# Kernel tuning notes

Hardware: AMD Instinct MI355X
Metric: run time of the kernel (lower is better)

## Reference

```python
import jax, jax.numpy as jnp
import numpy as np

HIDDEN = 2560
HEADS = 32
HEAD_DIM = HIDDEN // HEADS  # 80


def setup_inputs() -> dict:
    key = jax.random.key(0)
    ks = jax.random.split(key, 7)
    B, S, L = 2, 2048, 512
    scale = 1.0 / np.sqrt(HIDDEN)
    return {
        "hidden_states": jax.random.normal(ks[0], (B, S, HIDDEN), jnp.float32),
        "live_state": jax.random.normal(ks[1], (B, L, HIDDEN), jnp.float32),
        # nn.Linear weights stored [out, in]; y = x @ W.T
        "Wq": jax.random.normal(ks[2], (HIDDEN, HIDDEN), jnp.float32) * scale,
        "Wk": jax.random.normal(ks[3], (HIDDEN, HIDDEN), jnp.float32) * scale,
        "Wv": jax.random.normal(ks[4], (HIDDEN, HIDDEN), jnp.float32) * scale,
        "Wo": jax.random.normal(ks[5], (HIDDEN, HIDDEN), jnp.float32) * scale,
        "gate_param": jax.random.normal(ks[6], (), jnp.float32) * 0.1,
    }


def reference(hidden_states, live_state, Wq, Wk, Wv, Wo, gate_param):
    B, S, D = hidden_states.shape
    L = live_state.shape[1]
    H, Dh = HEADS, HEAD_DIM

    q = (hidden_states @ Wq.T).reshape(B, S, H, Dh).transpose(0, 2, 1, 3)  # [B,H,S,Dh]
    k = (live_state @ Wk.T).reshape(B, L, H, Dh).transpose(0, 2, 1, 3)    # [B,H,L,Dh]
    v = (live_state @ Wv.T).reshape(B, L, H, Dh).transpose(0, 2, 1, 3)    # [B,H,L,Dh]

    scale = 1.0 / np.sqrt(Dh)
    scores = jnp.einsum("bhsd,bhld->bhsl", q, k) * scale
    attn_weights = jax.nn.softmax(scores, axis=-1)                        # [B,H,S,L]
    attn_out = jnp.einsum("bhsl,bhld->bhsd", attn_weights, v)
    attn_out = attn_out.transpose(0, 2, 1, 3).reshape(B, S, D)
    attn_out = attn_out @ Wo.T

    gate = jnp.tanh(gate_param)
    output = gate * attn_out
    return output, attn_weights
```

## Files before the change

### kernel.cpp

```cpp
#include <hip/hip_runtime.h>
#include <hip/hip_fp16.h>
#include <cstdint>
#include <cstddef>

#define HID 2560
#define NH  32
#define DHD 80
#define DHP 96
#define NB  2
#define NS  2048
#define NL  512

typedef _Float16 half8_t __attribute__((ext_vector_type(8)));
typedef float f32x4_t __attribute__((ext_vector_type(4)));

__device__ __forceinline__ void gload_lds16(const __half* g, __half* l) {
  __builtin_amdgcn_global_load_lds(
      (const __attribute__((address_space(1))) unsigned int*)g,
      (__attribute__((address_space(3))) unsigned int*)l, 16, 0, 0);
}

__global__ __launch_bounds__(256) void cast_all(const float* __restrict__ X,
                                                const float* __restrict__ LS,
                                                const float* __restrict__ Wq,
                                                const float* __restrict__ Wk,
                                                const float* __restrict__ Wv,
                                                const float* __restrict__ Wo,
                                                __half* __restrict__ Xh,
                                                __half* __restrict__ Lh,
                                                __half* __restrict__ Wqh,
                                                __half* __restrict__ Wkh,
                                                __half* __restrict__ Wvh,
                                                __half* __restrict__ Woh,
                                                __half* __restrict__ Qa,
                                                __half* __restrict__ Ka) {
  const int nX = NB * NS * HID / 4, nL = NB * NL * HID / 4, nW = HID * HID / 4;
  const int ncast = nX + nL + 4 * nW;
  const int qrows = NB * NH * NS, krows = NB * NH * NL;
  const int total = ncast + qrows + krows;
  for (int i = blockIdx.x * 256 + threadIdx.x; i < total; i += gridDim.x * 256) {
    if (i < ncast) {
      const float* src; __half* dst; int off;
      if (i < nX) { src = X; dst = Xh; off = i; }
      else if (i < nX + nL) { src = LS; dst = Lh; off = i - nX; }
      else {
        int j = i - nX - nL;
        int w = j / nW; off = j - w * nW;
        src = (w == 0) ? Wq : (w == 1) ? Wk : (w == 2) ? Wv : Wo;
        dst = (w == 0) ? Wqh : (w == 1) ? Wkh : (w == 2) ? Wvh : Woh;
      }
      float4 v = ((const float4*)src)[off];
      union { __half h[4]; uint2 u; } r;
      r.h[0] = __float2half(v.x);
      r.h[1] = __float2half(v.y);
      r.h[2] = __float2half(v.z);
      r.h[3] = __float2half(v.w);
      ((uint2*)dst)[off] = r.u;
    } else {
      const int j = i - ncast;
      const uint4 z = {0, 0, 0, 0};
      uint4* p = (j < qrows)
          ? (uint4*)(Qa + (size_t)j * DHP + DHD)
          : (uint4*)(Ka + (size_t)(j - qrows) * DHP + DHD);
      p[0] = z; p[1] = z;
    }
  }
}

__device__ __forceinline__ void gemm256_core(const __half* A, const __half* Bt,
                                             int bm, int bn, __half* smem,
                                             f32x4_t (&acc)[8][4]) {
  const int K = HID;
  const int tid  = threadIdx.x;
  const int lane = tid & 63;
  const int wave = tid >> 6;
  const int wr = wave >> 2, wc = wave & 3;
  const int fr = lane & 15, kb = lane >> 4;

  const int sr = tid >> 3;
  const int sj = (tid & 7) ^ (sr & 7);
  const __half* gA = A  + (size_t)(bm * 256 + sr) * K + sj * 8;
  const __half* gB = Bt + (size_t)(bn * 256 + sr) * K + sj * 8;

  auto stage = [&](int h, int kt, int bank) {
    const __half* gbase = (h < 2) ? gA : gB;
    const int rbase = (h & 1) * 128;
#pragma unroll
    for (int i = 0; i < 2; ++i) {
      const __half* g = gbase + (size_t)(rbase + i * 64) * K + (size_t)kt * 64;
      __half* l = smem + bank * 32768 + (h < 2 ? 0 : 16384) + (rbase + i * 64) * 64 + tid * 8;
      gload_lds16(g, l);
    }
  };
  auto rdA = [&](int m, int kk, int bank) -> half8_t {
    const int row = wr * 128 + m * 16 + fr;
    const int off = row * 128 + ((kk * 64 + kb * 16) ^ ((fr & 7) << 4));
    return *(const half8_t*)((const char*)(smem + bank * 32768) + off);
  };
  auto rdB = [&](int n, int kk, int bank) -> half8_t {
    const int row = wc * 64 + n * 16 + fr;
    const int off = row * 128 + ((kk * 64 + kb * 16) ^ ((fr & 7) << 4));
    return *(const half8_t*)((const char*)(smem + bank * 32768 + 16384) + off);
  };

  half8_t af[4][2], bf[4][2];

#pragma unroll
  for (int h = 0; h < 4; ++h) stage(h, 0, 0);

  const int nk = K >> 6;
  for (int kt = 0; kt < nk; ++kt) {
    const int bk = kt & 1, nb2 = bk ^ 1;
    const bool pf = (kt + 1 < nk);

    if (pf) { stage(0, kt + 1, nb2); stage(1, kt + 1, nb2); }
    if (pf) asm volatile("s_waitcnt vmcnt(4)" ::: "memory");
    else    asm volatile("s_waitcnt vmcnt(0)" ::: "memory");
    asm volatile("s_barrier" ::: "memory");
#pragma unroll
    for (int m = 0; m < 4; ++m)
#pragma unroll
      for (int kk = 0; kk < 2; ++kk) af[m][kk] = rdA(m, kk, bk);
#pragma unroll
    for (int n = 0; n < 2; ++n)
#pragma unroll
      for (int kk = 0; kk < 2; ++kk) bf[n][kk] = rdB(n, kk, bk);
    __builtin_amdgcn_s_setprio(1);
#pragma unroll
    for (int m = 0; m < 4; ++m)
#pragma unroll
      for (int n = 0; n < 2; ++n)
#pragma unroll
        for (int kk = 0; kk < 2; ++kk)
          acc[m][n] = __builtin_amdgcn_mfma_f32_16x16x32_f16(af[m][kk], bf[n][kk], acc[m][n], 0, 0, 0);
    __builtin_amdgcn_s_setprio(0);
    asm volatile("s_barrier" ::: "memory");

#pragma unroll
    for (int n = 2; n < 4; ++n)
#pragma unroll
      for (int kk = 0; kk < 2; ++kk) bf[n][kk] = rdB(n, kk, bk);
    if (pf) stage(2, kt + 1, nb2);
    asm volatile("s_barrier" ::: "memory");
    __builtin_amdgcn_s_setprio(1);
#pragma unroll
    for (int m = 0; m < 4; ++m)
#pragma unroll
      for (int n = 2; n < 4; ++n)
#pragma unroll
        for (int kk = 0; kk < 2; ++kk)
          acc[m][n] = __builtin_amdgcn_mfma_f32_16x16x32_f16(af[m][kk], bf[n][kk], acc[m][n], 0, 0, 0);
    __builtin_amdgcn_s_setprio(0);
    asm volatile("s_barrier" ::: "memory");

#pragma unroll
    for (int m = 0; m < 4; ++m)
#pragma unroll
      for (int kk = 0; kk < 2; ++kk) af[m][kk] = rdA(m + 4, kk, bk);
    if (pf) stage(3, kt + 1, nb2);
    asm volatile("s_barrier" ::: "memory");
    __builtin_amdgcn_s_setprio(1);
#pragma unroll
    for (int m = 0; m < 4; ++m)
#pragma unroll
      for (int n = 2; n < 4; ++n)
#pragma unroll
        for (int kk = 0; kk < 2; ++kk)
          acc[m + 4][n] = __builtin_amdgcn_mfma_f32_16x16x32_f16(af[m][kk], bf[n][kk], acc[m + 4][n], 0, 0, 0);
    __builtin_amdgcn_s_setprio(0);
    asm volatile("s_barrier" ::: "memory");

    asm volatile("s_barrier" ::: "memory");
    __builtin_amdgcn_s_setprio(1);
#pragma unroll
    for (int m = 0; m < 4; ++m)
#pragma unroll
      for (int n = 0; n < 2; ++n)
#pragma unroll
        for (int kk = 0; kk < 2; ++kk)
          acc[m + 4][n] = __builtin_amdgcn_mfma_f32_16x16x32_f16(af[m][kk], bf[n][kk], acc[m + 4][n], 0, 0, 0);
    __builtin_amdgcn_s_setprio(0);
    asm volatile("s_barrier" ::: "memory");
  }
}

__global__ __launch_bounds__(512) void fused_qkv(const __half* __restrict__ X,
                                                 const __half* __restrict__ L,
                                                 const __half* __restrict__ Wq,
                                                 const __half* __restrict__ Wk,
                                                 const __half* __restrict__ Wv,
                                                 __half* __restrict__ Qa,
                                                 __half* __restrict__ Ka,
                                                 __half* __restrict__ Va) {
  __shared__ __half smem[2 * 32768];
  int wg = blockIdx.x;
  wg = (wg & 7) * 30 + (wg >> 3);

  int mode, bm, bn;
  const __half *A, *B;
  if (wg < 160)      { mode = 0; A = X; B = Wq; bm = wg / 10;        bn = wg - bm * 10; }
  else if (wg < 200) { mode = 1; A = L; B = Wk; bm = (wg - 160) / 10; bn = (wg - 160) - bm * 10; }
  else               { mode = 2; A = L; B = Wv; bm = (wg - 200) / 10; bn = (wg - 200) - bm * 10; }

  f32x4_t acc[8][4] = {};
  gemm256_core(A, B, bm, bn, smem, acc);

  const int lane = threadIdx.x & 63, wave = threadIdx.x >> 6;
  const int wr = wave >> 2, wc = wave & 3;
  const int fr = lane & 15, kb = lane >> 4;

#pragma unroll
  for (int m = 0; m < 8; ++m)
#pragma unroll
    for (int n = 0; n < 4; ++n)
#pragma unroll
      for (int r = 0; r < 4; ++r) {
        const int row = bm * 256 + wr * 128 + m * 16 + kb * 4 + r;
        const int col = bn * 256 + wc * 64 + n * 16 + fr;
        const float v = acc[m][n][r];
        const int h = col / DHD, d = col - h * DHD;
        if (mode == 0) {
          const int b = row >> 11, s = row & 2047;
          Qa[(((size_t)(b * NH + h)) * NS + s) * DHP + d] =
              __float2half(v * 0.11180339887498949f);
        } else if (mode == 1) {
          const int b = row >> 9, l = row & 511;
          Ka[(((size_t)(b * NH + h)) * NL + l) * DHP + d] = __float2half(v);
        } else {
          const int b = row >> 9, l = row & 511;
          Va[(((size_t)(b * NH + h)) * DHP + d) * NL + l] = __float2half(v);
        }
      }
}

__global__ __launch_bounds__(512) void gemm256_o(const __half* __restrict__ A,
                                                 const __half* __restrict__ Bt,
                                                 float* __restrict__ out,
                                                 const float* __restrict__ gate_p) {
  __shared__ __half smem[2 * 32768];
  int wg = blockIdx.x;
  wg = (wg & 7) * 20 + (wg >> 3);
  const int bm = wg / 10, bn = wg - bm * 10;

  f32x4_t acc[8][4] = {};
  gemm256_core(A, Bt, bm, bn, smem, acc);

  const float gate = tanhf(gate_p[0]);
  const int lane = threadIdx.x & 63, wave = threadIdx.x >> 6;
  const int wr = wave >> 2, wc = wave & 3;
  const int fr = lane & 15, kb = lane >> 4;

#pragma unroll
  for (int m = 0; m < 8; ++m)
#pragma unroll
    for (int n = 0; n < 4; ++n)
#pragma unroll
      for (int r = 0; r < 4; ++r) {
        const int row = bm * 256 + wr * 128 + m * 16 + kb * 4 + r;
        const int col = bn * 256 + wc * 64 + n * 16 + fr;
        out[(size_t)row * HID + col] = gate * acc[m][n][r];
      }
}

__global__ __launch_bounds__(256) void attn_kernel(const __half* __restrict__ Q,
                                                   const __half* __restrict__ Kt,
                                                   const __half* __restrict__ Vt,
                                                   float* __restrict__ P,
                                                   __half* __restrict__ AO) {
  __shared__ __half Pl[4 * 16 * 520];
  __shared__ __half KV[6144];
  const int tid = threadIdx.x;
  const int lane = tid & 63, wave = tid >> 6;
  const int fr = lane & 15, kb = lane >> 4;
  const int bh = blockIdx.y;
  const int r0 = blockIdx.x * 64 + wave * 16;

  const __half* Qb = Q  + ((size_t)bh * NS + r0) * DHP;
  const __half* Kb = Kt + (size_t)bh * NL * DHP;
  const __half* Vb = Vt + (size_t)bh * DHP * NL;

  half8_t aq[3];
#pragma unroll
  for (int kk = 0; kk < 3; ++kk)
    aq[kk] = *(const half8_t*)(Qb + (size_t)fr * DHP + kk * 32 + kb * 8);

  f32x4_t scr[32];

  for (int c = 0; c < 8; ++c) {
#pragma unroll
    for (int i = 0; i < 3; ++i) {
      const int s = (wave * 3 + i) * 64 + lane;
      gload_lds16(Kb + (size_t)c * 64 * DHP + s * 8, KV + s * 8);
    }
    __syncthreads();
#pragma unroll
    for (int ntl = 0; ntl < 4; ++ntl) {
      f32x4_t a = {};
#pragma unroll
      for (int kk = 0; kk < 3; ++kk) {
        half8_t bfv = *(const half8_t*)(KV + (ntl * 16 + fr) * DHP + kk * 32 + kb * 8);
        a = __builtin_amdgcn_mfma_f32_16x16x32_f16(aq[kk], bfv, a, 0, 0, 0);
      }
      scr[c * 4 + ntl] = a;
    }
    __syncthreads();
  }

  __half* Plw = Pl + wave * (16 * 520);
#pragma unroll
  for (int r = 0; r < 4; ++r) {
    float m = -1e30f;
#pragma unroll
    for (int nt = 0; nt < 32; ++nt) m = fmaxf(m, scr[nt][r]);
#pragma unroll
    for (int d = 1; d < 16; d <<= 1) m = fmaxf(m, __shfl_xor(m, d));
    float s = 0.f;
#pragma unroll
    for (int nt = 0; nt < 32; ++nt) {
      float p = __expf(scr[nt][r] - m);
      scr[nt][r] = p;
      s += p;
    }
#pragma unroll
    for (int d = 1; d < 16; d <<= 1) s += __shfl_xor(s, d);
    const float iv = 1.f / s;
    const int srow = r0 + kb * 4 + r;
    float* Pr = P + ((size_t)bh * NS + srow) * NL;
#pragma unroll
    for (int nt = 0; nt < 32; ++nt) {
      float p = scr[nt][r] * iv;
      Pr[nt * 16 + fr] = p;
      Plw[(kb * 4 + r) * 520 + nt * 16 + fr] = __float2half(p);
    }
  }

  f32x4_t oc[5] = {};
  for (int c = 0; c < 8; ++c) {
#pragma unroll
    for (int i = 0; i < 3; ++i) {
      const int s = (wave * 3 + i) * 64 + lane;
      int row = s / 9;
      int col = s - row * 9;
      if (row > 79) row = 79;
      if (col > 7) col = 7;
      gload_lds16(Vb + (size_t)row * NL + c * 64 + col * 8, KV + s * 8);
    }
    __syncthreads();
#pragma unroll
    for (int k0l = 0; k0l < 2; ++k0l) {
      half8_t ap = *(const half8_t*)(Plw + fr * 520 + (c * 2 + k0l) * 32 + kb * 8);
#pragma unroll
      for (int n = 0; n < 5; ++n) {
        half8_t bv = *(const half8_t*)(KV + (n * 16 + fr) * 72 + k0l * 32 + kb * 8);
        oc[n] = __builtin_amdgcn_mfma_f32_16x16x32_f16(ap, bv, oc[n], 0, 0, 0);
      }
    }
    __syncthreads();
  }

  const int b = bh >> 5, h = bh & 31;
#pragma unroll
  for (int n = 0; n < 5; ++n)
#pragma unroll
    for (int r = 0; r < 4; ++r) {
      const int srow = r0 + kb * 4 + r;
      AO[((size_t)b * NS + srow) * HID + h * DHD + n * 16 + fr] = __float2half(oc[n][r]);
    }
}

extern "C" void kernel_launch(void* const* d_in, const int* in_sizes, int n_in,
                              void* d_out, int out_size, void* d_ws, size_t ws_size,
                              hipStream_t stream) {
  const float* X  = (const float*)d_in[0];
  const float* LS = (const float*)d_in[1];
  const float* Wq = (const float*)d_in[2];
  const float* Wk = (const float*)d_in[3];
  const float* Wv = (const float*)d_in[4];
  const float* Wo = (const float*)d_in[5];
  const float* gp = (const float*)d_in[6];
  float* out  = (float*)d_out;
  float* Pout = out + (size_t)NB * NS * HID;

  char* w = (char*)d_ws;
  auto alloc = [&](size_t bytes) {
    char* p = w;
    w += (bytes + 255) & ~(size_t)255;
    return p;
  };
  __half* Xh  = (__half*)alloc((size_t)NB * NS * HID * 2);
  __half* Lh  = (__half*)alloc((size_t)NB * NL * HID * 2);
  __half* Wqh = (__half*)alloc((size_t)HID * HID * 2);
  __half* Wkh = (__half*)alloc((size_t)HID * HID * 2);
  __half* Wvh = (__half*)alloc((size_t)HID * HID * 2);
  __half* Woh = (__half*)alloc((size_t)HID * HID * 2);
  __half* Qa  = (__half*)alloc((size_t)NB * NH * NS * DHP * 2);
  __half* Ka  = (__half*)alloc((size_t)NB * NH * NL * DHP * 2);
  __half* Va  = (__half*)alloc((size_t)NB * NH * DHP * NL * 2);
  (void)alloc(4096);
  __half* AOh = Xh;

  cast_all<<<dim3(2048), dim3(256), 0, stream>>>(X, LS, Wq, Wk, Wv, Wo,
                                                 Xh, Lh, Wqh, Wkh, Wvh, Woh,
                                                 Qa, Ka);
  fused_qkv<<<dim3(240), dim3(512), 0, stream>>>(Xh, Lh, Wqh, Wkh, Wvh, Qa, Ka, Va);
  attn_kernel<<<dim3(NS / 64, NB * NH), dim3(256), 0, stream>>>(
      Qa, Ka, Va, Pout, AOh);
  gemm256_o<<<dim3(160), dim3(512), 0, stream>>>(AOh, Woh, out, gp);
}
```

Before: 325.3 us.

## Software-pipeline LDS fragment reads across K iterations in the GEMM main loop

Restructures the GEMM main loop so the first A/B fragments for the next K tile are read from LDS at the end of the current iteration. The vmcnt wait moves to the last phase, which lets global-to-LDS loads overlap more MFMA work. Stages 2 and 3 are now issued together. This aims to hide LDS and global load latency behind MFMA, at the cost of extra live registers for prefetched fragments and a reordered set of barrier hazards that could raise register pressure.

```diff
diff --git a/kernel.cpp b/kernel.cpp
--- a/kernel.cpp
+++ b/kernel.cpp
@@ -103,10 +103,20 @@
     return *(const half8_t*)((const char*)(smem + bank * 32768 + 16384) + off);
   };
 
-  half8_t af[4][2], bf[4][2];
+  half8_t af[4][2], bf01[2][2], bf23[2][2];
 
 #pragma unroll
   for (int h = 0; h < 4; ++h) stage(h, 0, 0);
+  asm volatile("s_waitcnt vmcnt(0)" ::: "memory");
+  asm volatile("s_barrier" ::: "memory");
+#pragma unroll
+  for (int m = 0; m < 4; ++m)
+#pragma unroll
+    for (int kk = 0; kk < 2; ++kk) af[m][kk] = rdA(m, kk, 0);
+#pragma unroll
+  for (int n = 0; n < 2; ++n)
+#pragma unroll
+    for (int kk = 0; kk < 2; ++kk) bf01[n][kk] = rdB(n, kk, 0);
 
   const int nk = K >> 6;
   for (int kt = 0; kt < nk; ++kt) {
@@ -114,17 +124,24 @@
     const bool pf = (kt + 1 < nk);
 
     if (pf) { stage(0, kt + 1, nb2); stage(1, kt + 1, nb2); }
-    if (pf) asm volatile("s_waitcnt vmcnt(4)" ::: "memory");
-    else    asm volatile("s_waitcnt vmcnt(0)" ::: "memory");
-    asm volatile("s_barrier" ::: "memory");
+    asm volatile("s_barrier" ::: "memory");
+    __builtin_amdgcn_s_setprio(1);
 #pragma unroll
     for (int m = 0; m < 4; ++m)
 #pragma unroll
-      for (int kk = 0; kk < 2; ++kk) af[m][kk] = rdA(m, kk, bk);
+      for (int n = 0; n < 2; ++n)
+#pragma unroll
+        for (int kk = 0; kk < 2; ++kk)
+          acc[m][n] = __builtin_amdgcn_mfma_f32_16x16x32_f16(af[m][kk], bf01[n][kk], acc[m][n], 0, 0, 0);
+    __builtin_amdgcn_s_setprio(0);
+    asm volatile("s_barrier" ::: "memory");
+
 #pragma unroll
     for (int n = 0; n < 2; ++n)
 #pragma unroll
-      for (int kk = 0; kk < 2; ++kk) bf[n][kk] = rdB(n, kk, bk);
+      for (int kk = 0; kk < 2; ++kk) bf23[n][kk] = rdB(n + 2, kk, bk);
+    if (pf) { stage(2, kt + 1, nb2); stage(3, kt + 1, nb2); }
+    asm volatile("s_barrier" ::: "memory");
     __builtin_amdgcn_s_setprio(1);
 #pragma unroll
     for (int m = 0; m < 4; ++m)
@@ -132,54 +149,47 @@
       for (int n = 0; n < 2; ++n)
 #pragma unroll
         for (int kk = 0; kk < 2; ++kk)
-          acc[m][n] = __builtin_amdgcn_mfma_f32_16x16x32_f16(af[m][kk], bf[n][kk], acc[m][n], 0, 0, 0);
+          acc[m][n + 2] = __builtin_amdgcn_mfma_f32_16x16x32_f16(af[m][kk], bf23[n][kk], acc[m][n + 2], 0, 0, 0);
     __builtin_amdgcn_s_setprio(0);
     asm volatile("s_barrier" ::: "memory");
 
 #pragma unroll
-    for (int n = 2; n < 4; ++n)
-#pragma unroll
-      for (int kk = 0; kk < 2; ++kk) bf[n][kk] = rdB(n, kk, bk);
-    if (pf) stage(2, kt + 1, nb2);
+    for (int m = 0; m < 4; ++m)
+#pragma unroll
+      for (int kk = 0; kk < 2; ++kk) af[m][kk] = rdA(m + 4, kk, bk);
     asm volatile("s_barrier" ::: "memory");
     __builtin_amdgcn_s_setprio(1);
 #pragma unroll
     for (int m = 0; m < 4; ++m)
 #pragma unroll
-      for (int n = 2; n < 4; ++n)
+      for (int n = 0; n < 2; ++n)
 #pragma unroll
         for (int kk = 0; kk < 2; ++kk)
-          acc[m][n] = __builtin_amdgcn_mfma_f32_16x16x32_f16(af[m][kk], bf[n][kk], acc[m][n], 0, 0, 0);
+          acc[m + 4][n] = __builtin_amdgcn_mfma_f32_16x16x32_f16(af[m][kk], bf01[n][kk], acc[m + 4][n], 0, 0, 0);
     __builtin_amdgcn_s_setprio(0);
     asm volatile("s_barrier" ::: "memory");
 
+    if (pf) asm volatile("s_waitcnt vmcnt(0)" ::: "memory");
+    asm volatile("s_barrier" ::: "memory");
+    __builtin_amdgcn_s_setprio(1);
 #pragma unroll
     for (int m = 0; m < 4; ++m)
 #pragma unroll
-      for (int kk = 0; kk < 2; ++kk) af[m][kk] = rdA(m + 4, kk, bk);
-    if (pf) stage(3, kt + 1, nb2);
-    asm volatile("s_barrier" ::: "memory");
-    __builtin_amdgcn_s_setprio(1);
-#pragma unroll
-    for (int m = 0; m < 4; ++m)
-#pragma unroll
-      for (int n = 2; n < 4; ++n)
+      for (int n = 0; n < 2; ++n)
 #pragma unroll
         for (int kk = 0; kk < 2; ++kk)
-          acc[m + 4][n] = __builtin_amdgcn_mfma_f32_16x16x32_f16(af[m][kk], bf[n][kk], acc[m + 4][n], 0, 0, 0);
+          acc[m + 4][n + 2] = __builtin_amdgcn_mfma_f32_16x16x32_f16(af[m][kk], bf23[n][kk], acc[m + 4][n + 2], 0, 0, 0);
     __builtin_amdgcn_s_setprio(0);
-    asm volatile("s_barrier" ::: "memory");
-
-    asm volatile("s_barrier" ::: "memory");
-    __builtin_amdgcn_s_setprio(1);
-#pragma unroll
-    for (int m = 0; m < 4; ++m)
+    if (pf) {
+#pragma unroll
+      for (int m = 0; m < 4; ++m)
+#pragma unroll
+        for (int kk = 0; kk < 2; ++kk) af[m][kk] = rdA(m, kk, nb2);
 #pragma unroll
       for (int n = 0; n < 2; ++n)
 #pragma unroll
-        for (int kk = 0; kk < 2; ++kk)
-          acc[m + 4][n] = __builtin_amdgcn_mfma_f32_16x16x32_f16(af[m][kk], bf[n][kk], acc[m + 4][n], 0, 0, 0);
-    __builtin_amdgcn_s_setprio(0);
+        for (int kk = 0; kk < 2; ++kk) bf01[n][kk] = rdB(n, kk, nb2);
+    }
     asm volatile("s_barrier" ::: "memory");
   }
 }
```

New measurement: 335.9 us. 1.03x slower.
